# Kernel tuning notes

Hardware: AMD Instinct MI355X
Metric: run time of the kernel (lower is better)

The kernel has to match this reference:

```python
import jax, jax.numpy as jnp
import numpy as np

EPS = 1e-12  # matches torch F.normalize default eps


def _l2_normalize(x):
    # torch F.normalize(x, dim=2): x / max(||x||_2, eps)
    n = jnp.sqrt(jnp.sum(x * x, axis=2, keepdims=True))
    return x / jnp.maximum(n, EPS)


def setup_inputs() -> dict:
    key = jax.random.key(0)
    k1, k2 = jax.random.split(key)
    B, C, HW = 8, 1024, 3136
    fm_s = jax.random.normal(k1, (B, C, HW), dtype=jnp.float32)
    fm_t = jax.random.normal(k2, (B, C, HW), dtype=jnp.float32)
    return {"fm_s": fm_s, "fm_t": fm_t}


def reference(fm_s, fm_t):
    s = _l2_normalize(fm_s)  # (B, C, HW)
    t = _l2_normalize(fm_t)  # (B, C, HW)
    # poly_kernel(a, b) = (a[:,None,:,:] * b[:,:,None,:]).sum(-1)**2
    # == (b @ a^T)**2 computed as a batched matmul -> (B, C, C)
    k_ss = jnp.einsum('bnc,bmc->bnm', s, s) ** 2
    k_st = jnp.einsum('bnc,bmc->bnm', t, s) ** 2
    return jnp.mean(k_ss) - 2.0 * jnp.mean(k_st)
```

## Files before the change

### kernel.cpp

```cpp
#include <hip/hip_runtime.h>
#include <stdint.h>

typedef __attribute__((ext_vector_type(4)))  int   i32x4;
typedef __attribute__((ext_vector_type(8)))  int   i32x8;
typedef __attribute__((ext_vector_type(16))) float f32x16;

#define NB 8
#define NC 1024
#define NHW 3136
#define ROWB8 3200
#define NKT 25

__device__ inline float sq4(float4 v){
  return fmaf(v.x,v.x, fmaf(v.y,v.y, fmaf(v.z,v.z, v.w*v.w)));
}

__device__ __forceinline__ void load_lds16(const void* g, void* l){
  __builtin_amdgcn_global_load_lds(
      (const __attribute__((address_space(1))) unsigned int*)g,
      (__attribute__((address_space(3))) unsigned int*)l,
      16, 0, 0);
}

__device__ __forceinline__ f32x16 MFS(i32x8 a, i32x8 b, f32x16 c){
  return __builtin_amdgcn_mfma_scale_f32_32x32x64_f8f6f4(
      a, b, c, 0, 0, 0, 0x7F7F7F7F, 0, 0x7F7F7F7F);
}

__device__ __forceinline__ i32x8 rdfrag(const char* base, int cLo, int cHi){
  i32x4 lo = *(const i32x4*)(base + cLo);
  i32x4 hi = *(const i32x4*)(base + cHi);
  return __builtin_shufflevector(lo, hi, 0,1,2,3,4,5,6,7);
}

__device__ __forceinline__ int cvt4(float4 v, float s){
  int pk = __builtin_amdgcn_cvt_pk_fp8_f32(v.x*s, v.y*s, 0,  0);
  pk     = __builtin_amdgcn_cvt_pk_fp8_f32(v.z*s, v.w*s, pk, 1);
  return pk;
}

__device__ __forceinline__ void loadRow(const float* src, int l, float4* v){
  const float4* p = (const float4*)src;
  #pragma unroll
  for (int j = 0; j < 12; j++) v[j] = p[l + 64*j];
  v[12] = (l < 16) ? p[768 + l] : make_float4(0.f,0.f,0.f,0.f);
}

__device__ __forceinline__ void finRow(const float4* v, char* dst, int l){
  float ssq = 0.f;
  #pragma unroll
  for (int j = 0; j < 13; j++) ssq += sq4(v[j]);
  #pragma unroll
  for (int off = 32; off; off >>= 1) ssq += __shfl_xor(ssq, off);
  const float inv = 32.0f / fmaxf(sqrtf(ssq), 1e-12f);
  #pragma unroll
  for (int j = 0; j < 12; j++)
    *(int*)(dst + 4*(l + 64*j)) = cvt4(v[j], inv);
  if (l < 16)      *(int*)(dst + 3072 + 4*l) = cvt4(v[12], inv);
  else if (l < 20) *(int4*)(dst + 3136 + 16*(l-16)) = make_int4(0,0,0,0);
}

__global__ __launch_bounds__(256, 4) void k_norm(const float* __restrict__ s,
                                                 const float* __restrict__ t,
                                                 char* __restrict__ Sn,
                                                 char* __restrict__ Tn,
                                                 float* __restrict__ accbuf){
  if (blockIdx.x == 0 && threadIdx.x == 0){
    accbuf[0] = 0.f; accbuf[1] = 0.f;
    ((int*)accbuf)[2] = 0;
  }
  const int gw = (blockIdx.x << 2) | (threadIdx.x >> 6);
  const int l  = threadIdx.x & 63;
  const bool isS = (gw < 4096);
  const int r0 = (isS ? gw : gw - 4096) * 2;
  const float* base = (isS ? s : t) + (size_t)r0 * NHW;
  char*        ob   = (isS ? Sn : Tn) + (size_t)r0 * ROWB8;

  float4 v0[13], v1[13];
  loadRow(base,        l, v0);
  loadRow(base + NHW,  l, v1);
  finRow(v0, ob,         l);
  finRow(v1, ob + ROWB8, l);
}


#define BAR   __builtin_amdgcn_s_barrier()
#define LGKM0 asm volatile("s_waitcnt lgkmcnt(0)" ::: "memory")
#define LGKM8 asm volatile("s_waitcnt lgkmcnt(8)" ::: "memory")
#define VM6   asm volatile("s_waitcnt vmcnt(6)" ::: "memory")
#define SB0   __builtin_amdgcn_sched_barrier(0)
#define PRIO1 __builtin_amdgcn_s_setprio(1)
#define PRIO0 __builtin_amdgcn_s_setprio(0)

#define ISSUE(MAT, D, H, KT) do{ \
  const char* _g = ((MAT)? gB : gA) + (KT)*128 + (H)*(128*ROWB8); \
  char* _d = ldsw + (D)*65536 + (MAT)*32768 + (H)*16384; \
  load_lds16(_g,              _d); \
  load_lds16(_g + 64*ROWB8,   _d + 8192); \
}while(0)

#define RDA(D, MH) do{ \
  const char* _a = aRow + (D) + (MH)*8192; \
  af[0][0] = rdfrag(_a,        c00, c01); \
  af[0][1] = rdfrag(_a,        c10, c11); \
  af[1][0] = rdfrag(_a + 4096, c00, c01); \
  af[1][1] = rdfrag(_a + 4096, c10, c11); \
}while(0)

#define RDB(D, NH) do{ \
  const char* _b = bRow + (D) + (NH)*4096; \
  bf[NH][0] = rdfrag(_b, c00, c01); \
  bf[NH][1] = rdfrag(_b, c10, c11); \
}while(0)

#define MMQ(MH, NH) do{ \
  acc[((MH)*2+0)*2+(NH)] = MFS(af[0][0], bf[NH][0], acc[((MH)*2+0)*2+(NH)]); \
  acc[((MH)*2+1)*2+(NH)] = MFS(af[1][0], bf[NH][0], acc[((MH)*2+1)*2+(NH)]); \
  acc[((MH)*2+0)*2+(NH)] = MFS(af[0][1], bf[NH][1], acc[((MH)*2+0)*2+(NH)]); \
  acc[((MH)*2+1)*2+(NH)] = MFS(af[1][1], bf[NH][1], acc[((MH)*2+1)*2+(NH)]); \
}while(0)

__global__ __launch_bounds__(512,2) void k_gemm(const char* __restrict__ Sn,
                                                const char* __restrict__ Tn,
                                                float* __restrict__ accbuf,
                                                float* __restrict__ out){
  __shared__ char lds[131072];
  const int tid = threadIdx.x;
  const int l   = tid & 63;
  const int w   = tid >> 6;
  const int wr  = w >> 2;
  const int wc  = w & 3;

  const int b   = blockIdx.x & 7;
  const int idx = blockIdx.x >> 3;
  int tm, tn, which; float wgt;
  if (idx < 16){ which = 1; tm = idx >> 2; tn = idx & 3; wgt = 1.f; }
  else {
    int e = idx - 16; which = 0;
    if      (e < 4){ tm = 0; tn = e;   }
    else if (e < 7){ tm = 1; tn = e-3; }
    else if (e < 9){ tm = 2; tn = e-5; }
    else           { tm = 3; tn = 3;   }
    wgt = (tm == tn) ? 1.f : 2.f;
  }
  const char* Ab = (which ? Tn : Sn) + (size_t)b*(NC*ROWB8) + (size_t)tm*(256*ROWB8);
  const char* Bb = Sn                + (size_t)b*(NC*ROWB8) + (size_t)tn*(256*ROWB8);

  const int scol = ((l & 7) << 4) ^ ((l >> 3) << 4);
  const char* gA = Ab + (8*w + (l >> 3))*ROWB8 + scol;
  const char* gB = Bb + (8*w + (l >> 3))*ROWB8 + scol;
  char* ldsw = lds + w*1024;

  const int swz = (l & 7) << 4;
  const int cg  = 32*(l >> 5);
  const int c00 = ( cg           ) ^ swz;
  const int c01 = ( cg | 16      ) ^ swz;
  const int c10 = ( cg | 64      ) ^ swz;
  const int c11 = ( cg | 64 | 16 ) ^ swz;
  const char* aRow = lds +         (wr*128 + (l & 31))*128;
  const char* bRow = lds + 32768 + (wc*64  + (l & 31))*128;

  i32x8 af[2][2], bf[2][2];
  f32x16 acc[8];
  #pragma unroll
  for (int i = 0; i < 8; i++) acc[i] = (f32x16){};

  ISSUE(1,0,0,0); ISSUE(1,0,1,0); ISSUE(0,0,0,0); ISSUE(0,0,1,0);
  ISSUE(1,1,0,1); ISSUE(1,1,1,1); ISSUE(0,1,0,1);
  VM6; BAR;

  for (int i = 0; i < 12; i++){
    const int t1 = 2*i + 1;
    const int t2 = 2*i + 2;
    int t3 = 2*i + 3; if (t3 > 24) t3 = 24;

    RDA(0,0); RDB(0,0);
    ISSUE(0,1,1,t1);
    LGKM8; BAR; LGKM0; SB0; PRIO1; MMQ(0,0); PRIO0; BAR;
    RDB(0,1);
    BAR; LGKM0; SB0; PRIO1; MMQ(0,1); PRIO0; BAR;
    RDA(0,1);
    ISSUE(1,0,0,t2); ISSUE(1,0,1,t2);
    BAR; LGKM0; SB0; PRIO1; MMQ(1,0); PRIO0; BAR;
    ISSUE(0,0,0,t2);
    BAR; PRIO1; MMQ(1,1); PRIO0; VM6; BAR;

    RDA(65536,0); RDB(65536,0);
    ISSUE(0,0,1,t2);
    LGKM8; BAR; LGKM0; SB0; PRIO1; MMQ(0,0); PRIO0; BAR;
    RDB(65536,1);
    BAR; LGKM0; SB0; PRIO1; MMQ(0,1); PRIO0; BAR;
    RDA(65536,1);
    ISSUE(1,1,0,t3); ISSUE(1,1,1,t3);
    BAR; LGKM0; SB0; PRIO1; MMQ(1,0); PRIO0; BAR;
    ISSUE(0,1,0,t3);
    BAR; PRIO1; MMQ(1,1); PRIO0; VM6; BAR;
  }

  RDA(0,0); RDB(0,0); RDB(0,1);
  MMQ(0,0); MMQ(0,1);
  RDA(0,1);
  MMQ(1,0); MMQ(1,1);

  float p = 0.f;
  #pragma unroll
  for (int f = 0; f < 8; f++)
    #pragma unroll
    for (int e = 0; e < 16; e++)
      p = fmaf(acc[f][e], acc[f][e], p);
  #pragma unroll
  for (int off = 32; off; off >>= 1) p += __shfl_down(p, off);
  __syncthreads();
  float* red = (float*)lds;
  if (l == 0) red[w] = p;
  __syncthreads();
  if (tid == 0){
    float sum = red[0]+red[1]+red[2]+red[3]+red[4]+red[5]+red[6]+red[7];
    atomicAdd(&accbuf[which], wgt * sum);
    __threadfence();
    int old = atomicAdd((int*)accbuf + 2, 1);
    if (old == 207){
      float a0 = atomicAdd(&accbuf[0], 0.f);
      float a1 = atomicAdd(&accbuf[1], 0.f);
      out[0] = (a0 - 2.0f*a1) * 1.1368683772161603e-13f;
    }
  }
}

extern "C" void kernel_launch(void* const* d_in, const int* in_sizes, int n_in,
                              void* d_out, int out_size, void* d_ws, size_t ws_size,
                              hipStream_t stream){
  const float* fs = (const float*)d_in[0];
  const float* ft = (const float*)d_in[1];
  float* out = (float*)d_out;
  float* accbuf = (float*)d_ws;
  char* Sn = (char*)d_ws + 256;
  char* Tn = Sn + (size_t)NB*NC*ROWB8;

  k_norm<<<dim3(2048), dim3(256), 0, stream>>>(fs, ft, Sn, Tn, accbuf);
  k_gemm<<<dim3(208), dim3(512), 0, stream>>>(Sn, Tn, accbuf, out);
}
```

Measured before the change: 90.25 us.

## Fuse normalization and GEMM into one persistent kernel with per-batch readiness counters

```diff
diff --git a/kernel.cpp b/kernel.cpp
--- a/kernel.cpp
+++ b/kernel.cpp
@@ -9,7 +9,6 @@
 #define NC 1024
 #define NHW 3136
 #define ROWB8 3200
-#define NKT 25
 
 __device__ inline float sq4(float4 v){
   return fmaf(v.x,v.x, fmaf(v.y,v.y, fmaf(v.z,v.z, v.w*v.w)));
@@ -45,7 +44,6 @@
   for (int j = 0; j < 12; j++) v[j] = p[l + 64*j];
   v[12] = (l < 16) ? p[768 + l] : make_float4(0.f,0.f,0.f,0.f);
 }
-
 __device__ __forceinline__ void finRow(const float4* v, char* dst, int l){
   float ssq = 0.f;
   #pragma unroll
@@ -60,29 +58,9 @@
   else if (l < 20) *(int4*)(dst + 3136 + 16*(l-16)) = make_int4(0,0,0,0);
 }
 
-__global__ __launch_bounds__(256, 4) void k_norm(const float* __restrict__ s,
-                                                 const float* __restrict__ t,
-                                                 char* __restrict__ Sn,
-                                                 char* __restrict__ Tn,
-                                                 float* __restrict__ accbuf){
-  if (blockIdx.x == 0 && threadIdx.x == 0){
-    accbuf[0] = 0.f; accbuf[1] = 0.f;
-    ((int*)accbuf)[2] = 0;
-  }
-  const int gw = (blockIdx.x << 2) | (threadIdx.x >> 6);
-  const int l  = threadIdx.x & 63;
-  const bool isS = (gw < 4096);
-  const int r0 = (isS ? gw : gw - 4096) * 2;
-  const float* base = (isS ? s : t) + (size_t)r0 * NHW;
-  char*        ob   = (isS ? Sn : Tn) + (size_t)r0 * ROWB8;
-
-  float4 v0[13], v1[13];
-  loadRow(base,        l, v0);
-  loadRow(base + NHW,  l, v1);
-  finRow(v0, ob,         l);
-  finRow(v1, ob + ROWB8, l);
-}
-
+__global__ void k_zero(int* w){
+  if (threadIdx.x < 16) w[threadIdx.x] = 0;
+}
 
 #define BAR   __builtin_amdgcn_s_barrier()
 #define LGKM0 asm volatile("s_waitcnt lgkmcnt(0)" ::: "memory")
@@ -120,19 +98,64 @@
   acc[((MH)*2+1)*2+(NH)] = MFS(af[1][1], bf[NH][1], acc[((MH)*2+1)*2+(NH)]); \
 }while(0)
 
-__global__ __launch_bounds__(512,2) void k_gemm(const char* __restrict__ Sn,
-                                                const char* __restrict__ Tn,
-                                                float* __restrict__ accbuf,
-                                                float* __restrict__ out){
+__global__ __launch_bounds__(512,2) void k_fused(const float* __restrict__ s,
+                                                 const float* __restrict__ t,
+                                                 char* __restrict__ Sn,
+                                                 char* __restrict__ Tn,
+                                                 float* __restrict__ accbuf,
+                                                 float* __restrict__ out){
   __shared__ char lds[131072];
+  const int i   = blockIdx.x;
   const int tid = threadIdx.x;
   const int l   = tid & 63;
-  const int w   = tid >> 6;
+  const int wv  = tid >> 6;
+  int* cnt  = (int*)accbuf + 4;
+  int* done = (int*)accbuf + 12;
+
+  const int jb = (i < 208) ? (i & 7) : 7;
+  for (int b = 0; b <= jb; b++){
+    const int P = 256 - 26*b;
+    int r;
+    if (i < 208){
+      const int res = i & 7;
+      r = (i >> 3)*(8 - b) + (res > b ? res - b : 0);
+    } else {
+      r = 26*(8 - b) + (i - 208);
+    }
+    const int start = (r*2048)/P;
+    const int end   = ((r+1)*2048)/P;
+    for (int idx = start + wv; idx < end; idx += 8){
+      const int off = idx & 1023;
+      const bool isS = (idx < 1024);
+      const int gr = b*1024 + off;
+      const float* src = (isS ? s : t) + (size_t)gr * NHW;
+      char*        dst = (isS ? Sn : Tn) + (size_t)gr * ROWB8;
+      float4 v[13];
+      loadRow(src, l, v);
+      finRow(v, dst, l);
+    }
+    __syncthreads();
+    if (tid == 0){
+      __threadfence();
+      __hip_atomic_fetch_add(&cnt[b], end - start,
+                             __ATOMIC_RELEASE, __HIP_MEMORY_SCOPE_AGENT);
+    }
+  }
+  if (i >= 208) return;
+
+  if (tid == 0){
+    while (__hip_atomic_load(&cnt[jb], __ATOMIC_RELAXED,
+                             __HIP_MEMORY_SCOPE_AGENT) < 2048)
+      __builtin_amdgcn_s_sleep(8);
+    (void)__hip_atomic_load(&cnt[jb], __ATOMIC_ACQUIRE,
+                            __HIP_MEMORY_SCOPE_AGENT);
+  }
+  __syncthreads();
+
+  const int w   = wv;
   const int wr  = w >> 2;
   const int wc  = w & 3;
-
-  const int b   = blockIdx.x & 7;
-  const int idx = blockIdx.x >> 3;
+  const int idx = i >> 3;
   int tm, tn, which; float wgt;
   if (idx < 16){ which = 1; tm = idx >> 2; tn = idx & 3; wgt = 1.f; }
   else {
@@ -143,8 +166,8 @@
     else           { tm = 3; tn = 3;   }
     wgt = (tm == tn) ? 1.f : 2.f;
   }
-  const char* Ab = (which ? Tn : Sn) + (size_t)b*(NC*ROWB8) + (size_t)tm*(256*ROWB8);
-  const char* Bb = Sn                + (size_t)b*(NC*ROWB8) + (size_t)tn*(256*ROWB8);
+  const char* Ab = (which ? Tn : Sn) + (size_t)jb*(NC*ROWB8) + (size_t)tm*(256*ROWB8);
+  const char* Bb = Sn                + (size_t)jb*(NC*ROWB8) + (size_t)tn*(256*ROWB8);
 
   const int scol = ((l & 7) << 4) ^ ((l >> 3) << 4);
   const char* gA = Ab + (8*w + (l >> 3))*ROWB8 + scol;
@@ -163,16 +186,16 @@
   i32x8 af[2][2], bf[2][2];
   f32x16 acc[8];
   #pragma unroll
-  for (int i = 0; i < 8; i++) acc[i] = (f32x16){};
+  for (int k = 0; k < 8; k++) acc[k] = (f32x16){};
 
   ISSUE(1,0,0,0); ISSUE(1,0,1,0); ISSUE(0,0,0,0); ISSUE(0,0,1,0);
   ISSUE(1,1,0,1); ISSUE(1,1,1,1); ISSUE(0,1,0,1);
   VM6; BAR;
 
-  for (int i = 0; i < 12; i++){
-    const int t1 = 2*i + 1;
-    const int t2 = 2*i + 2;
-    int t3 = 2*i + 3; if (t3 > 24) t3 = 24;
+  for (int it = 0; it < 12; it++){
+    const int t1 = 2*it + 1;
+    const int t2 = 2*it + 2;
+    int t3 = 2*it + 3; if (t3 > 24) t3 = 24;
 
     RDA(0,0); RDB(0,0);
     ISSUE(0,1,1,t1);
@@ -218,7 +241,7 @@
     float sum = red[0]+red[1]+red[2]+red[3]+red[4]+red[5]+red[6]+red[7];
     atomicAdd(&accbuf[which], wgt * sum);
     __threadfence();
-    int old = atomicAdd((int*)accbuf + 2, 1);
+    int old = atomicAdd(done, 1);
     if (old == 207){
       float a0 = atomicAdd(&accbuf[0], 0.f);
       float a1 = atomicAdd(&accbuf[1], 0.f);
@@ -237,6 +260,6 @@
   char* Sn = (char*)d_ws + 256;
   char* Tn = Sn + (size_t)NB*NC*ROWB8;
 
-  k_norm<<<dim3(2048), dim3(256), 0, stream>>>(fs, ft, Sn, Tn, accbuf);
-  k_gemm<<<dim3(208), dim3(512), 0, stream>>>(Sn, Tn, accbuf, out);
-}
+  k_zero<<<1, 64, 0, stream>>>((int*)d_ws);
+  k_fused<<<dim3(256), dim3(512), 0, stream>>>(fs, ft, Sn, Tn, accbuf, out);
+}
```

Result: slower. 216.6 us (+140.0%).
